# Optimization experiments

Measured on AMD Instinct MI355X. Metric: run time of the kernel, lower is better.

Reference implementation:

```python
import jax, jax.numpy as jnp
import numpy as np

HID = 256
N, D, K, EPOCHS = 100000, 512, 5, 2


def _lin(x, w, b):
    return x @ w.T + b


def setup_inputs() -> dict:
    key = jax.random.key(0)
    ks = jax.random.split(key, 16)
    s = 0.05
    return {
        "x0": jax.random.normal(ks[0], (N, D), jnp.float32),
        "x1": jax.random.normal(ks[1], (N, D), jnp.float32),
        "Hin0_w": jax.random.normal(ks[2], (HID, D), jnp.float32) * s,
        "Hin0_b": jax.random.normal(ks[3], (HID,), jnp.float32) * s,
        "Hin1_w": jax.random.normal(ks[4], (HID, D), jnp.float32) * s,
        "Hin1_b": jax.random.normal(ks[5], (HID,), jnp.float32) * s,
        "w0_w": jax.random.normal(ks[6], (HID, HID), jnp.float32) * s,
        "w0_b": jax.random.normal(ks[7], (HID,), jnp.float32) * s,
        "w1_w": jax.random.normal(ks[8], (HID, HID), jnp.float32) * s,
        "w1_b": jax.random.normal(ks[9], (HID,), jnp.float32) * s,
        "w2_w": jax.random.normal(ks[10], (HID, HID), jnp.float32) * s,
        "w2_b": jax.random.normal(ks[11], (HID,), jnp.float32) * s,
        "edge0": jax.random.randint(ks[12], (2, N * K), 0, N, dtype=jnp.int32),
        "edge1": jax.random.randint(ks[13], (2, N * K), 0, N, dtype=jnp.int32),
        "k": K,
        "update_epoch": EPOCHS,
    }


def reference(x0, x1, Hin0_w, Hin0_b, Hin1_w, Hin1_b, w0_w, w0_b,
              w1_w, w1_b, w2_w, w2_b, edge0, edge1, k, update_epoch):
    xs = (x0, x1)
    edges = (edge0, edge1)
    Hws = ((Hin0_w, Hin0_b), (Hin1_w, Hin1_b))
    n_views = len(xs)

    # per-view input projections: h_init[v] = H_ins[v](train_view[v])
    h_inits = [_lin(x, w, b) for x, (w, b) in zip(xs, Hws)]

    finals = []
    for v in range(n_views):
        # neighbor table: node i's k neighbors are edge[1][i*k : (i+1)*k]
        nbr_idx = edges[v][1].reshape(-1, k)  # [N, k]
        # cross-view self term: mean over other views of w2(h_init_other)
        slf = _lin(h_inits[1 - v], w2_w, w2_b)  # [N, HID] (nv-1 == 1)
        h = h_inits[v]
        for _ in range(update_epoch):
            h = _lin(h, w0_w, w0_b)
            # mean_j w1(h[nbr_j]) == w1(mean_j h[nbr_j]) since w1 is affine
            nbr_mean = h[nbr_idx].mean(axis=1)  # [N, HID] gather + reduce
            h = h + _lin(nbr_mean, w1_w, w1_b) + slf
        finals.append(jax.nn.relu(h))

    # average final embeddings across views
    h_out = sum(finals) / n_views
    return h_out
```

## Files before the change

kernel.cpp:

```cpp
#include <hip/hip_runtime.h>

#define NN 100000
#define DD 512
#define HH 256
#define KNB 5

typedef __attribute__((ext_vector_type(8))) short short8v;
typedef __attribute__((ext_vector_type(4))) short short4v;
typedef __attribute__((ext_vector_type(4))) float float4v;

static __device__ __forceinline__ float bf2f(unsigned short u) {
  union { unsigned int i; float f; } c;
  c.i = ((unsigned int)u) << 16;
  return c.f;
}
static __device__ __forceinline__ unsigned short f2bf(float f) {
  union { float f; unsigned int i; } c;
  c.f = f;
  unsigned int u = c.i;
  u += 0x7FFFu + ((u >> 16) & 1u);
  return (unsigned short)(u >> 16);
}

#define GLOAD16(g, l) __builtin_amdgcn_global_load_lds( \
    (const __attribute__((address_space(1))) unsigned int*)(g), \
    (__attribute__((address_space(3))) unsigned int*)(l), 16, 0, 0)

__global__ void cvt2(const float* __restrict__ s0, short* __restrict__ d0,
                     const float* __restrict__ s1, short* __restrict__ d1) {
  const int S1 = (HH * DD) / 4;
  int i = blockIdx.x * blockDim.x + threadIdx.x;
  if (i >= 2 * S1) return;
  const float* s = (i < S1) ? s0 : s1;
  short* d = (i < S1) ? d0 : d1;
  int j = (i < S1) ? i : i - S1;
  float4 v = reinterpret_cast<const float4*>(s)[j];
  short4v o;
  o[0] = (short)f2bf(v.x); o[1] = (short)f2bf(v.y);
  o[2] = (short)f2bf(v.z); o[3] = (short)f2bf(v.w);
  reinterpret_cast<short4v*>(d)[j] = o;
}

__global__ void prep_w01(const float* __restrict__ w0, const float* __restrict__ w1,
                         const float* __restrict__ w2, const float* __restrict__ b0,
                         const float* __restrict__ b1, const float* __restrict__ b2,
                         short* __restrict__ Bcat, float* __restrict__ bc) {
  int i = blockIdx.x;
  int j = threadIdx.x;
  Bcat[(size_t)i * 768 + j]       = (short)f2bf(w0[i * 256 + j]);
  Bcat[(size_t)i * 768 + 512 + j] = (short)f2bf(w2[i * 256 + j]);
  float acc = 0.f;
  for (int k = 0; k < 256; ++k)
    acc = fmaf(w1[i * 256 + k], w0[k * 256 + j], acc);
  Bcat[(size_t)i * 768 + 256 + j] = (short)f2bf(acc);
  if (j == 0) {
    float s = b0[i] + b1[i] + b2[i];
    for (int k = 0; k < 256; ++k) s = fmaf(w1[i * 256 + k], b0[k], s);
    bc[i] = s;
  }
}

__global__ __launch_bounds__(512, 6) void proj_k(
    const float* __restrict__ Af0, const float* __restrict__ Af1,
    const short* __restrict__ Bw0, const short* __restrict__ Bw1,
    const float* __restrict__ bi0, const float* __restrict__ bi1,
    short* __restrict__ Cb0, short* __restrict__ Cb1)
{
  const float* Af = blockIdx.y ? Af1 : Af0;
  const short* Bw = blockIdx.y ? Bw1 : Bw0;
  const float* bias = blockIdx.y ? bi1 : bi0;
  short* Cb = blockIdx.y ? Cb1 : Cb0;

  __shared__ __align__(16) char BsRaw[256 * 64 * 2];
  __shared__ __align__(16) char AsRaw[64 * 64 * 4];

  const int tid = threadIdx.x;
  const int lane = tid & 63;
  const int wave = tid >> 6;
  const int wr = wave >> 2;
  const int wc = wave & 3;
  const int row0 = blockIdx.x * 64;

  float4v acc[2][4];
#pragma unroll
  for (int m = 0; m < 2; ++m)
#pragma unroll
    for (int n = 0; n < 4; ++n) acc[m][n] = (float4v)0.f;

  for (int k0 = 0; k0 < DD; k0 += 64) {
#pragma unroll
    for (int q = 0; q < 4; ++q) {
      int ch = q * 512 + tid;
      int r = ch >> 3, pc = ch & 7;
      int lc = pc ^ (r & 7);
      GLOAD16(Bw + (size_t)r * DD + k0 + lc * 8, BsRaw + (q * 512 + wave * 64) * 16);
    }
#pragma unroll
    for (int q = 0; q < 2; ++q) {
      int ch = q * 512 + tid;
      int r = ch >> 4, pc = ch & 15;
      int lc = pc ^ (r & 15);
      int rg = min(row0 + r, NN - 1);
      GLOAD16(Af + (size_t)rg * DD + k0 + lc * 4, AsRaw + (q * 512 + wave * 64) * 16);
    }
    __syncthreads();

#pragma unroll
    for (int kk = 0; kk < 2; ++kk) {
      const int ckb = kk * 4 + (lane >> 4);
      short8v a[2], b[4];
#pragma unroll
      for (int n = 0; n < 4; ++n) {
        int rb = wc * 64 + n * 16 + (lane & 15);
        b[n] = *reinterpret_cast<const short8v*>(BsRaw + rb * 128 + ((ckb ^ (rb & 7)) << 4));
      }
#pragma unroll
      for (int m = 0; m < 2; ++m) {
        int ra = wr * 32 + m * 16 + (lane & 15);
        int ck0 = kk * 8 + (lane >> 4) * 2;
        float4v f0 = *reinterpret_cast<const float4v*>(AsRaw + ra * 256 + ((ck0 ^ (ra & 15)) << 4));
        float4v f1 = *reinterpret_cast<const float4v*>(AsRaw + ra * 256 + (((ck0 + 1) ^ (ra & 15)) << 4));
        short8v av;
        av[0] = (short)f2bf(f0[0]); av[1] = (short)f2bf(f0[1]);
        av[2] = (short)f2bf(f0[2]); av[3] = (short)f2bf(f0[3]);
        av[4] = (short)f2bf(f1[0]); av[5] = (short)f2bf(f1[1]);
        av[6] = (short)f2bf(f1[2]); av[7] = (short)f2bf(f1[3]);
        a[m] = av;
      }
#pragma unroll
      for (int m = 0; m < 2; ++m)
#pragma unroll
        for (int n = 0; n < 4; ++n)
          acc[m][n] = __builtin_amdgcn_mfma_f32_16x16x32_bf16(b[n], a[m], acc[m][n], 0, 0, 0);
    }
    __syncthreads();
  }

  const int crow = lane & 15;
  const int cg = (lane >> 4) * 4;
#pragma unroll
  for (int m = 0; m < 2; ++m) {
    int rg = row0 + wr * 32 + m * 16 + crow;
    if (rg >= NN) continue;
#pragma unroll
    for (int n = 0; n < 4; ++n) {
      int colb = wc * 64 + n * 16 + cg;
      size_t off = (size_t)rg * HH + colb;
      float4v bi = *reinterpret_cast<const float4v*>(bias + colb);
      short4v o;
#pragma unroll
      for (int i = 0; i < 4; ++i) o[i] = (short)f2bf(acc[m][n][i] + bi[i]);
      *reinterpret_cast<short4v*>(Cb + off) = o;
    }
  }
}

template<int EPI>
__global__ __launch_bounds__(512, 4) void epoch_k(
    const short* __restrict__ D, const short* __restrict__ Cc,
    const short* __restrict__ Bw, const float* __restrict__ bias,
    short* __restrict__ Ob, float* __restrict__ Of,
    const short* __restrict__ Fin, const int* __restrict__ nbr)
{
  __shared__ __align__(16) char BsRaw[256 * 64 * 2];
  __shared__ __align__(16) char AsRaw[128 * 64 * 2];
  __shared__ int nbrL[128][KNB];

  const int tid = threadIdx.x;
  const int lane = tid & 63;
  const int wave = tid >> 6;
  const int wr = wave >> 2;
  const int wc = wave & 3;
  const int row0 = blockIdx.x * 128;

  for (int e = tid; e < 128 * KNB; e += 512) {
    int r = e / KNB;
    int rg = min(row0 + r, NN - 1);
    nbrL[r][e - r * KNB] = nbr[rg * KNB + (e - r * KNB)];
  }

  float4v acc[4][4];
#pragma unroll
  for (int m = 0; m < 4; ++m)
#pragma unroll
    for (int n = 0; n < 4; ++n) acc[m][n] = (float4v)0.f;

  for (int k0 = 0; k0 < 768; k0 += 64) {
#pragma unroll
    for (int q = 0; q < 4; ++q) {
      int ch = q * 512 + tid;
      int r = ch >> 3, pc = ch & 7;
      int lc = pc ^ (r & 7);
      GLOAD16(Bw + (size_t)r * 768 + k0 + lc * 8, BsRaw + (q * 512 + wave * 64) * 16);
    }
    if (k0 < 256 || k0 >= 512) {
      const short* H = (k0 < 256) ? (D + k0) : (Cc + (k0 - 512));
#pragma unroll
      for (int q = 0; q < 2; ++q) {
        int ch = q * 512 + tid;
        int r = ch >> 3, pc = ch & 7;
        int lc = pc ^ (r & 7);
        int rg = min(row0 + r, NN - 1);
        GLOAD16(H + (size_t)rg * HH + lc * 8, AsRaw + (q * 512 + wave * 64) * 16);
      }
    } else {
      const int kb = k0 - 256;
#pragma unroll
      for (int q = 0; q < 2; ++q) {
        int ch = q * 512 + tid;
        int r = ch >> 3, pc = ch & 7;
        int lc = pc ^ (r & 7);
        float a8[8] = {0.f, 0.f, 0.f, 0.f, 0.f, 0.f, 0.f, 0.f};
#pragma unroll
        for (int j = 0; j < KNB; ++j) {
          int id = nbrL[r][j];
          short8v v = *reinterpret_cast<const short8v*>(D + (size_t)id * HH + kb + lc * 8);
#pragma unroll
          for (int x = 0; x < 8; ++x) a8[x] += bf2f((unsigned short)v[x]);
        }
        short8v o;
#pragma unroll
        for (int x = 0; x < 8; ++x) o[x] = (short)f2bf(a8[x] * 0.2f);
        *reinterpret_cast<short8v*>(AsRaw + ch * 16) = o;
      }
    }
    __syncthreads();

#pragma unroll
    for (int kk = 0; kk < 2; ++kk) {
      const int ckb = kk * 4 + (lane >> 4);
      short8v a[4], b[4];
#pragma unroll
      for (int n = 0; n < 4; ++n) {
        int rb = wc * 64 + n * 16 + (lane & 15);
        b[n] = *reinterpret_cast<const short8v*>(BsRaw + rb * 128 + ((ckb ^ (rb & 7)) << 4));
      }
#pragma unroll
      for (int m = 0; m < 4; ++m) {
        int ra = wr * 64 + m * 16 + (lane & 15);
        a[m] = *reinterpret_cast<const short8v*>(AsRaw + ra * 128 + ((ckb ^ (ra & 7)) << 4));
      }
#pragma unroll
      for (int m = 0; m < 4; ++m)
#pragma unroll
        for (int n = 0; n < 4; ++n)
          acc[m][n] = __builtin_amdgcn_mfma_f32_16x16x32_bf16(b[n], a[m], acc[m][n], 0, 0, 0);
    }
    __syncthreads();
  }

  const int crow = lane & 15;
  const int cg = (lane >> 4) * 4;
#pragma unroll
  for (int m = 0; m < 4; ++m) {
    int rg = row0 + wr * 64 + m * 16 + crow;
    if (rg >= NN) continue;
#pragma unroll
    for (int n = 0; n < 4; ++n) {
      int colb = wc * 64 + n * 16 + cg;
      size_t off = (size_t)rg * HH + colb;
      float4v bi = *reinterpret_cast<const float4v*>(bias + colb);
      float v[4];
#pragma unroll
      for (int i = 0; i < 4; ++i) v[i] = acc[m][n][i] + bi[i];
      if constexpr (EPI >= 2) {
#pragma unroll
        for (int i = 0; i < 4; ++i) v[i] = fmaxf(v[i], 0.f);
      }
      if constexpr (EPI <= 2) {
        short4v o;
#pragma unroll
        for (int i = 0; i < 4; ++i) o[i] = (short)f2bf(v[i]);
        *reinterpret_cast<short4v*>(Ob + off) = o;
      } else {
        short4v f4 = *reinterpret_cast<const short4v*>(Fin + off);
        float4v o;
#pragma unroll
        for (int i = 0; i < 4; ++i)
          o[i] = (v[i] + bf2f((unsigned short)f4[i])) * 0.5f;
        *reinterpret_cast<float4v*>(Of + off) = o;
      }
    }
  }
}

extern "C" void kernel_launch(void* const* d_in, const int* in_sizes, int n_in,
                              void* d_out, int out_size, void* d_ws, size_t ws_size,
                              hipStream_t stream) {
  const float* x0  = (const float*)d_in[0];
  const float* x1  = (const float*)d_in[1];
  const float* wh0 = (const float*)d_in[2];
  const float* bh0 = (const float*)d_in[3];
  const float* wh1 = (const float*)d_in[4];
  const float* bh1 = (const float*)d_in[5];
  const float* w0  = (const float*)d_in[6];
  const float* b0  = (const float*)d_in[7];
  const float* w1  = (const float*)d_in[8];
  const float* b1  = (const float*)d_in[9];
  const float* w2  = (const float*)d_in[10];
  const float* b2  = (const float*)d_in[11];
  const int* e0    = (const int*)d_in[12];
  const int* e1    = (const int*)d_in[13];
  const int* nbr0  = e0 + (size_t)NN * KNB;
  const int* nbr1  = e1 + (size_t)NN * KNB;
  float* out       = (float*)d_out;

  char* ws = (char*)d_ws;
  size_t off = 0;
  auto alloc = [&](size_t bytes) -> void* {
    off = (off + 255) & ~(size_t)255;
    void* p = ws + off;
    off += bytes;
    return p;
  };

  short* Wh0  = (short*)alloc((size_t)HH * DD * 2);
  short* Wh1  = (short*)alloc((size_t)HH * DD * 2);
  short* Bcat = (short*)alloc((size_t)HH * 768 * 2);
  float* bc   = (float*)alloc((size_t)HH * 4);
  const size_t NB = (size_t)NN * HH * 2;
  short* hi0 = (short*)alloc(NB);
  short* hi1 = (short*)alloc(NB);
  short* hb0 = (short*)alloc(NB);
  short* hb1 = (short*)alloc(NB);
  short* f0  = (short*)alloc(NB);

  cvt2<<<dim3(256), dim3(256), 0, stream>>>(wh0, Wh0, wh1, Wh1);
  prep_w01<<<dim3(256), dim3(256), 0, stream>>>(w0, w1, w2, b0, b1, b2, Bcat, bc);

  proj_k<<<dim3((NN + 63) / 64, 2), dim3(512), 0, stream>>>(
      x0, x1, Wh0, Wh1, bh0, bh1, hi0, hi1);

  dim3 ge((NN + 127) / 128);

  epoch_k<0><<<ge, dim3(512), 0, stream>>>(hi0, hi1, Bcat, bc, hb0, nullptr, nullptr, nbr0);
  epoch_k<0><<<ge, dim3(512), 0, stream>>>(hi1, hi0, Bcat, bc, hb1, nullptr, nullptr, nbr1);

  epoch_k<2><<<ge, dim3(512), 0, stream>>>(hb0, hi1, Bcat, bc, f0, nullptr, nullptr, nbr0);
  epoch_k<3><<<ge, dim3(512), 0, stream>>>(hb1, hi0, Bcat, bc, nullptr, out, f0, nbr1);

  (void)in_sizes; (void)n_in; (void)out_size; (void)ws_size;
}
```

Before: 539.5 us.

## Convert fp32 activations to bf16 at LDS store time in projection kernel

The projection kernel used to copy raw fp32 A tiles into LDS with global_load_lds and convert them to bf16 inside the MFMA loop. Each thread now does a register load of 8 floats, converts once, and writes a swizzled bf16 chunk into LDS, which halves the A tile's LDS footprint and removes repeated conversions. Occupancy hints rise for proj_k (6 to 8) and epoch_k (4 to 6). The trade is that the async direct-to-LDS load becomes a synchronous register round trip, and the tighter launch bounds may cause register spills.

```diff
diff --git a/kernel.cpp b/kernel.cpp
--- a/kernel.cpp
+++ b/kernel.cpp
@@ -60,7 +60,7 @@
   }
 }
 
-__global__ __launch_bounds__(512, 6) void proj_k(
+__global__ __launch_bounds__(512, 8) void proj_k(
     const float* __restrict__ Af0, const float* __restrict__ Af1,
     const short* __restrict__ Bw0, const short* __restrict__ Bw1,
     const float* __restrict__ bi0, const float* __restrict__ bi1,
@@ -72,7 +72,7 @@
   short* Cb = blockIdx.y ? Cb1 : Cb0;
 
   __shared__ __align__(16) char BsRaw[256 * 64 * 2];
-  __shared__ __align__(16) char AsRaw[64 * 64 * 4];
+  __shared__ __align__(16) char AsRaw[64 * 64 * 2];
 
   const int tid = threadIdx.x;
   const int lane = tid & 63;
@@ -81,6 +81,11 @@
   const int wc = wave & 3;
   const int row0 = blockIdx.x * 64;
 
+  const int sr = tid >> 3;
+  const int spc = tid & 7;
+  const int slc = spc ^ (sr & 7);
+  const int srg = min(row0 + sr, NN - 1);
+
   float4v acc[2][4];
 #pragma unroll
   for (int m = 0; m < 2; ++m)
@@ -95,13 +100,16 @@
       int lc = pc ^ (r & 7);
       GLOAD16(Bw + (size_t)r * DD + k0 + lc * 8, BsRaw + (q * 512 + wave * 64) * 16);
     }
-#pragma unroll
-    for (int q = 0; q < 2; ++q) {
-      int ch = q * 512 + tid;
-      int r = ch >> 4, pc = ch & 15;
-      int lc = pc ^ (r & 15);
-      int rg = min(row0 + r, NN - 1);
-      GLOAD16(Af + (size_t)rg * DD + k0 + lc * 4, AsRaw + (q * 512 + wave * 64) * 16);
+    {
+      const float* src = Af + (size_t)srg * DD + k0 + slc * 8;
+      float4 f0 = *reinterpret_cast<const float4*>(src);
+      float4 f1 = *reinterpret_cast<const float4*>(src + 4);
+      short8v o;
+      o[0] = (short)f2bf(f0.x); o[1] = (short)f2bf(f0.y);
+      o[2] = (short)f2bf(f0.z); o[3] = (short)f2bf(f0.w);
+      o[4] = (short)f2bf(f1.x); o[5] = (short)f2bf(f1.y);
+      o[6] = (short)f2bf(f1.z); o[7] = (short)f2bf(f1.w);
+      *reinterpret_cast<short8v*>(AsRaw + tid * 16) = o;
     }
     __syncthreads();
 
@@ -117,15 +125,7 @@
 #pragma unroll
       for (int m = 0; m < 2; ++m) {
         int ra = wr * 32 + m * 16 + (lane & 15);
-        int ck0 = kk * 8 + (lane >> 4) * 2;
-        float4v f0 = *reinterpret_cast<const float4v*>(AsRaw + ra * 256 + ((ck0 ^ (ra & 15)) << 4));
-        float4v f1 = *reinterpret_cast<const float4v*>(AsRaw + ra * 256 + (((ck0 + 1) ^ (ra & 15)) << 4));
-        short8v av;
-        av[0] = (short)f2bf(f0[0]); av[1] = (short)f2bf(f0[1]);
-        av[2] = (short)f2bf(f0[2]); av[3] = (short)f2bf(f0[3]);
-        av[4] = (short)f2bf(f1[0]); av[5] = (short)f2bf(f1[1]);
-        av[6] = (short)f2bf(f1[2]); av[7] = (short)f2bf(f1[3]);
-        a[m] = av;
+        a[m] = *reinterpret_cast<const short8v*>(AsRaw + ra * 128 + ((ckb ^ (ra & 7)) << 4));
       }
 #pragma unroll
       for (int m = 0; m < 2; ++m)
@@ -156,7 +156,7 @@
 }
 
 template<int EPI>
-__global__ __launch_bounds__(512, 4) void epoch_k(
+__global__ __launch_bounds__(512, 6) void epoch_k(
     const short* __restrict__ D, const short* __restrict__ Cc,
     const short* __restrict__ Bw, const float* __restrict__ bias,
     short* __restrict__ Ob, float* __restrict__ Of,
```

Measured after the change: 1.695 ms. +214.1%, slower.
